# Kernel tuning notes

Measured on AMD Instinct MI355X. Metric: run time of the kernel, lower is better.

## Reference

```python
import jax, jax.numpy as jnp
import numpy as np

B, N, E, D, P = 128, 50000, 300000, 256, 8


def setup_inputs() -> dict:
    key = jax.random.key(0)
    ks = jax.random.split(key, 13)
    scale = 1.0 / np.sqrt(D)  # keep uniform-init logits numerically sane
    return {
        "instruction_batch": jax.random.normal(ks[0], (B, D), jnp.float32),
        "distribution": jax.random.uniform(ks[1], (N,), jnp.float32),
        "node_prop_similarities": jax.random.uniform(ks[2], (B, P), jnp.float32),
        "relation_similarity": jax.random.uniform(ks[3], (B,), jnp.float32),
        "node_attrs": jax.random.normal(ks[4], (N, D), jnp.float32),
        "edge_attrs": jax.random.normal(ks[5], (E, D), jnp.float32),
        "W_node_props": jax.random.uniform(ks[6], (P, D, D), jnp.float32) * scale,
        "W_edge": jax.random.uniform(ks[7], (D, D), jnp.float32) * scale,
        "w_node_score": jax.random.uniform(ks[8], (D,), jnp.float32) * scale,
        "w_rel_score": jax.random.uniform(ks[9], (D,), jnp.float32) * scale,
        "node_indices": jnp.sort(jax.random.randint(ks[10], (N,), 0, B)),
        "edge_batch_indices": jax.random.randint(ks[11], (E,), 0, B),
        "edge_indices": jax.random.randint(ks[12], (2, E), 0, N),
    }


def _segment_softmax(logits, seg, num_segments):
    # softmax over all entries sharing the same segment (= per-graph softmax)
    m = jax.ops.segment_max(logits, seg, num_segments=num_segments)
    e = jnp.exp(logits - m[seg])
    s = jax.ops.segment_sum(e, seg, num_segments=num_segments)
    return e / s[seg]


def reference(instruction_batch, distribution, node_prop_similarities,
              relation_similarity, node_attrs, edge_attrs,
              W_node_props, W_edge, w_node_score, w_rel_score,
              node_indices, edge_batch_indices, edge_indices):
    num_graphs = instruction_batch.shape[0]

    # node_scores[n,d] = elu( sum_p sim[n,p] * instr[n,d] * (W_p @ attr_n)[d] )
    sim_n = node_prop_similarities[node_indices]          # [N, P]
    instr_n = instruction_batch[node_indices]             # [N, D]
    wa = jnp.einsum("pde,ne->npd", W_node_props, node_attrs)  # [N, P, D]
    node_scores = jax.nn.elu(
        jnp.einsum("np,nd,npd->nd", sim_n, instr_n, wa))   # [N, D]

    # edge_scores[e,d] = elu( instr[batch(e),d] * (W_edge @ edge_attr_e)[d] )
    edge_scores = jax.nn.elu(
        instruction_batch[edge_batch_indices] * (edge_attrs @ W_edge.T))  # [E, D]

    # per-graph (sparse) softmax over node state logits
    state_logits = node_scores @ w_node_score              # [N]
    next_states = _segment_softmax(state_logits, node_indices, num_graphs)

    # scatter: aggregate weighted edge messages at destination nodes
    src, dst = edge_indices[0], edge_indices[1]
    msgs = distribution[src, None] * edge_scores           # [E, D]
    agg = jnp.zeros_like(node_scores).at[dst].add(msgs)    # [N, D]
    rel_logits = agg @ w_rel_score                         # [N]
    next_relations = _segment_softmax(rel_logits, node_indices, num_graphs)

    r = relation_similarity[node_indices]                  # [N]
    return r * next_relations + (1.0 - r) * next_states
```

## Files before the change

### kernel.cpp

```cpp
#include <hip/hip_runtime.h>

#define NB 128
#define NN 50000
#define NE 300000
#define ND 256
#define NP 8

typedef __attribute__((ext_vector_type(4))) float f32x4;
typedef __attribute__((ext_vector_type(8))) short s16x8;

__device__ __forceinline__ unsigned short bf16rtn(float f) {
    unsigned int u = __float_as_uint(f);
    unsigned int r = (u + 0x7fffu + ((u >> 16) & 1u)) >> 16;
    return (unsigned short)r;
}

__device__ __forceinline__ int cvtpk(float lo, float hi) {
    int r;
    asm("v_cvt_pk_bf16_f32 %0, %1, %2" : "=v"(r) : "v"(lo), "v"(hi));
    return r;
}

__device__ __forceinline__ s16x8 pack8(f32x4 a, f32x4 b) {
    union { int d[4]; s16x8 v; } u;
    u.d[0] = cvtpk(a[0], a[1]);
    u.d[1] = cvtpk(a[2], a[3]);
    u.d[2] = cvtpk(b[0], b[1]);
    u.d[3] = cvtpk(b[2], b[3]);
    return u.v;
}

__device__ __forceinline__ float eluf(float x) {
    return x > 0.f ? x : __expf(x) - 1.f;
}

__device__ __forceinline__ float rowsum16(float x) {
    int t;
    t = __builtin_amdgcn_update_dpp(0, __float_as_int(x), 0x121, 0xf, 0xf, true);
    x += __int_as_float(t);
    t = __builtin_amdgcn_update_dpp(0, __float_as_int(x), 0x122, 0xf, 0xf, true);
    x += __int_as_float(t);
    t = __builtin_amdgcn_update_dpp(0, __float_as_int(x), 0x124, 0xf, 0xf, true);
    x += __int_as_float(t);
    t = __builtin_amdgcn_update_dpp(0, __float_as_int(x), 0x128, 0xf, 0xf, true);
    x += __int_as_float(t);
    return x;
}

__device__ __forceinline__ void stage_W(char* Wl, const unsigned short* Wsrc,
                                        int tid, int nthr) {
    for (int i = tid; i < 8192; i += nthr) {
        int cg = i >> 9;
        int kk = (i >> 6) & 7;
        int ln = i & 63;
        const unsigned short* src =
            Wsrc + (size_t)(cg * 16 + (ln & 15)) * ND + kk * 32 + (ln >> 4) * 8;
        *(s16x8*)(Wl + i * 16) = *(const s16x8*)src;
    }
}

__global__ __launch_bounds__(256) void k_prep(
    const float* __restrict__ We, unsigned short* __restrict__ Wbf,
    const float* __restrict__ sim, const float* __restrict__ Wp,
    unsigned short* __restrict__ Weff,
    const int* __restrict__ nidx, int* __restrict__ starts,
    float* __restrict__ rel_logits,
    const int* __restrict__ eidx, const float* __restrict__ dist,
    float* __restrict__ dscg)
{
    int bid = blockIdx.x;
    int tid = threadIdx.x;
    if (bid < 64) {
        int i = (bid * 256 + tid) * 4;
        f32x4 v = *(const f32x4*)(We + i);
        Wbf[i + 0] = bf16rtn(v[0]); Wbf[i + 1] = bf16rtn(v[1]);
        Wbf[i + 2] = bf16rtn(v[2]); Wbf[i + 3] = bf16rtn(v[3]);
    } else if (bid < 320) {
        int wb = bid - 64;
        int chunk = (wb & 31) * 256 + tid;
        int off = chunk * 8;
        float wp[NP][8];
#pragma unroll
        for (int p = 0; p < NP; ++p) {
            const float* src = Wp + (size_t)p * ND * ND + off;
            f32x4 w0 = *(const f32x4*)src;
            f32x4 w1 = *(const f32x4*)(src + 4);
            wp[p][0] = w0[0]; wp[p][1] = w0[1]; wp[p][2] = w0[2]; wp[p][3] = w0[3];
            wp[p][4] = w1[0]; wp[p][5] = w1[1]; wp[p][6] = w1[2]; wp[p][7] = w1[3];
        }
        int b0 = (wb >> 5) * 16;
        for (int bb = 0; bb < 16; ++bb) {
            int b = b0 + bb;
            float g[8] = {0.f, 0.f, 0.f, 0.f, 0.f, 0.f, 0.f, 0.f};
#pragma unroll
            for (int p = 0; p < NP; ++p) {
                float s = sim[b * NP + p];
#pragma unroll
                for (int j = 0; j < 8; ++j) g[j] += s * wp[p][j];
            }
            s16x8 v;
#pragma unroll
            for (int j = 0; j < 8; ++j) v[j] = (short)bf16rtn(g[j]);
            *(s16x8*)(Weff + (size_t)b * ND * ND + off) = v;
        }
    } else {
        int n = (bid - 320) * 256 + tid;
        if (n < NE) dscg[n] = dist[eidx[n]];
        if (n >= NN) return;
        rel_logits[n] = 0.f;
        int cur = nidx[n];
        int prev = (n == 0) ? -1 : nidx[n - 1];
        for (int b2 = prev + 1; b2 <= cur; ++b2) starts[b2] = n;
        if (n == NN - 1)
            for (int b2 = cur + 1; b2 <= NB; ++b2) starts[b2] = NN;
    }
}

__global__ __launch_bounds__(1024, 4) void k_main(
    const float* __restrict__ instr, const float* __restrict__ dscg,
    const float* __restrict__ eattrs, const unsigned short* __restrict__ Wbf,
    const float* __restrict__ wrs, const int* __restrict__ ebidx,
    const int* __restrict__ eidx, float* __restrict__ rel_logits,
    const unsigned short* __restrict__ Weff, const float* __restrict__ nattrs,
    const float* __restrict__ wns, const int* __restrict__ starts,
    float* __restrict__ state_logits)
{
    __shared__ char Wl[131072];

    int tid = threadIdx.x;
    int lane = tid & 63;
    int wave = tid >> 6;
    int l15 = lane & 15;
    int q = lane >> 4;

    if (blockIdx.x < 256) {
        stage_W(Wl, Wbf, tid, 1024);
        __syncthreads();

        int gw = wave * 256 + blockIdx.x;
        const int NT = NE / 16;
        for (int t = gw; t < NT; t += 4096) {
            int e0 = t * 16;
            int e4 = e0 + 4 * q;
            int eb0 = ebidx[e4 + 0], eb1 = ebidx[e4 + 1];
            int eb2 = ebidx[e4 + 2], eb3 = ebidx[e4 + 3];
            float dv0 = dscg[e4 + 0], dv1 = dscg[e4 + 1];
            float dv2 = dscg[e4 + 2], dv3 = dscg[e4 + 3];
            int dd0 = eidx[NE + e4 + 0], dd1 = eidx[NE + e4 + 1];
            int dd2 = eidx[NE + e4 + 2], dd3 = eidx[NE + e4 + 3];

            const float* ib0 = instr + (size_t)eb0 * ND + l15;
            const float* ib1 = instr + (size_t)eb1 * ND + l15;
            const float* ib2 = instr + (size_t)eb2 * ND + l15;
            const float* ib3 = instr + (size_t)eb3 * ND + l15;

            const float* arow = eattrs + (size_t)(e0 + l15) * ND + q * 8;
            s16x8 afr[8];
#pragma unroll
            for (int kk = 0; kk < 8; ++kk) {
                f32x4 a0 = *(const f32x4*)(arow + kk * 32);
                f32x4 a1 = *(const f32x4*)(arow + kk * 32 + 4);
                afr[kk] = pack8(a0, a1);
            }

            float nv0 = ib0[0], nv1 = ib1[0], nv2 = ib2[0], nv3 = ib3[0];
            float nw = wrs[l15];

            float p0 = 0.f, p1 = 0.f, p2 = 0.f, p3 = 0.f;
#pragma unroll 1
            for (int cg = 0; cg < 16; ++cg) {
                float v0 = nv0, v1 = nv1, v2 = nv2, v3 = nv3, wvc = nw;
                int cn = (cg + 1 < 16 ? cg + 1 : 15) * 16;
                nv0 = ib0[cn]; nv1 = ib1[cn]; nv2 = ib2[cn]; nv3 = ib3[cn];
                nw = wrs[cn + l15];

                f32x4 acc = {0.f, 0.f, 0.f, 0.f};
                const char* fb = Wl + cg * 8192 + lane * 16;
                __builtin_amdgcn_s_setprio(1);
#pragma unroll
                for (int kk = 0; kk < 8; ++kk) {
                    s16x8 bf = *(const s16x8*)(fb + kk * 1024);
                    acc = __builtin_amdgcn_mfma_f32_16x16x32_bf16(afr[kk], bf, acc, 0, 0, 0);
                }
                __builtin_amdgcn_s_setprio(0);
                p0 += wvc * eluf(v0 * acc[0]);
                p1 += wvc * eluf(v1 * acc[1]);
                p2 += wvc * eluf(v2 * acc[2]);
                p3 += wvc * eluf(v3 * acc[3]);
            }
            p0 = rowsum16(p0); p1 = rowsum16(p1);
            p2 = rowsum16(p2); p3 = rowsum16(p3);
            if (l15 == 0) {
                atomicAdd(&rel_logits[dd0], dv0 * p0);
                atomicAdd(&rel_logits[dd1], dv1 * p1);
                atomicAdd(&rel_logits[dd2], dv2 * p2);
                atomicAdd(&rel_logits[dd3], dv3 * p3);
            }
        }
    } else {
        int nb = blockIdx.x - 256;
        int b = nb >> 1;
        int half = nb & 1;
        int s0 = starts[b], s1 = starts[b + 1];
        int nt = (s1 - s0 + 15) >> 4;

        stage_W(Wl, Weff + (size_t)b * ND * ND, tid, 1024);
        __syncthreads();

        const float* irow = instr + (size_t)b * ND + l15;
        for (int t = half * 16 + wave; t < nt; t += 32) {
            int n0 = s0 + t * 16;
            int arn = n0 + l15;
            bool valid = arn < s1;
            const float* arow = nattrs + (size_t)arn * ND + q * 8;
            s16x8 afr[8];
#pragma unroll
            for (int kk = 0; kk < 8; ++kk) {
                f32x4 a0 = {0.f, 0.f, 0.f, 0.f}, a1 = {0.f, 0.f, 0.f, 0.f};
                if (valid) {
                    a0 = *(const f32x4*)(arow + kk * 32);
                    a1 = *(const f32x4*)(arow + kk * 32 + 4);
                }
                afr[kk] = pack8(a0, a1);
            }

            float p0 = 0.f, p1 = 0.f, p2 = 0.f, p3 = 0.f;
#pragma unroll 1
            for (int cg = 0; cg < 16; ++cg) {
                f32x4 acc = {0.f, 0.f, 0.f, 0.f};
                const char* fb = Wl + cg * 8192 + lane * 16;
                __builtin_amdgcn_s_setprio(1);
#pragma unroll
                for (int kk = 0; kk < 8; ++kk) {
                    s16x8 bf = *(const s16x8*)(fb + kk * 1024);
                    acc = __builtin_amdgcn_mfma_f32_16x16x32_bf16(afr[kk], bf, acc, 0, 0, 0);
                }
                __builtin_amdgcn_s_setprio(0);
                int c = cg * 16;
                float ivc = irow[c];
                float wvc = wns[c + l15];
                p0 += wvc * eluf(ivc * acc[0]);
                p1 += wvc * eluf(ivc * acc[1]);
                p2 += wvc * eluf(ivc * acc[2]);
                p3 += wvc * eluf(ivc * acc[3]);
            }
            p0 = rowsum16(p0); p1 = rowsum16(p1);
            p2 = rowsum16(p2); p3 = rowsum16(p3);
            if (l15 == 0) {
                int n = n0 + 4 * q;
                if (n + 0 < s1) state_logits[n + 0] = p0;
                if (n + 1 < s1) state_logits[n + 1] = p1;
                if (n + 2 < s1) state_logits[n + 2] = p2;
                if (n + 3 < s1) state_logits[n + 3] = p3;
            }
        }
    }
}

__global__ __launch_bounds__(256) void k_softmax_mix(
    const float* __restrict__ state_l, const float* __restrict__ rel_l,
    const int* __restrict__ starts, const float* __restrict__ relsim,
    float* __restrict__ out)
{
    __shared__ float wms[4], wmr[4], wss[4], wsr[4];
    int b = blockIdx.x;
    int s0 = starts[b], s1 = starts[b + 1];
    if (s1 <= s0) return;
    int tid = threadIdx.x, lane = tid & 63, wave = tid >> 6;

    float ms = -3.4e38f, mr = -3.4e38f;
    for (int n = s0 + tid; n < s1; n += 256) {
        ms = fmaxf(ms, state_l[n]);
        mr = fmaxf(mr, rel_l[n]);
    }
#pragma unroll
    for (int m = 1; m < 64; m <<= 1) {
        ms = fmaxf(ms, __shfl_xor(ms, m, 64));
        mr = fmaxf(mr, __shfl_xor(mr, m, 64));
    }
    if (lane == 0) { wms[wave] = ms; wmr[wave] = mr; }
    __syncthreads();
    ms = fmaxf(fmaxf(wms[0], wms[1]), fmaxf(wms[2], wms[3]));
    mr = fmaxf(fmaxf(wmr[0], wmr[1]), fmaxf(wmr[2], wmr[3]));

    float ss = 0.f, sr = 0.f;
    for (int n = s0 + tid; n < s1; n += 256) {
        ss += __expf(state_l[n] - ms);
        sr += __expf(rel_l[n] - mr);
    }
#pragma unroll
    for (int m = 1; m < 64; m <<= 1) {
        ss += __shfl_xor(ss, m, 64);
        sr += __shfl_xor(sr, m, 64);
    }
    if (lane == 0) { wss[wave] = ss; wsr[wave] = sr; }
    __syncthreads();
    ss = wss[0] + wss[1] + wss[2] + wss[3];
    sr = wsr[0] + wsr[1] + wsr[2] + wsr[3];

    float rb = relsim[b];
    float iss = 1.f / ss, isr = 1.f / sr;
    for (int n = s0 + tid; n < s1; n += 256) {
        out[n] = rb * __expf(rel_l[n] - mr) * isr
               + (1.f - rb) * __expf(state_l[n] - ms) * iss;
    }
}

extern "C" void kernel_launch(void* const* d_in, const int* in_sizes, int n_in,
                              void* d_out, int out_size, void* d_ws, size_t ws_size,
                              hipStream_t stream) {
    const float* instr  = (const float*)d_in[0];
    const float* dist   = (const float*)d_in[1];
    const float* sim    = (const float*)d_in[2];
    const float* relsim = (const float*)d_in[3];
    const float* nattr  = (const float*)d_in[4];
    const float* eattr  = (const float*)d_in[5];
    const float* Wp     = (const float*)d_in[6];
    const float* We     = (const float*)d_in[7];
    const float* wns    = (const float*)d_in[8];
    const float* wrs    = (const float*)d_in[9];
    const int* nidx     = (const int*)d_in[10];
    const int* ebidx    = (const int*)d_in[11];
    const int* eidx     = (const int*)d_in[12];
    float* out = (float*)d_out;

    char* ws = (char*)d_ws;
    float* rel_logits   = (float*)ws;
    float* state_logits = rel_logits + NN;
    int* starts         = (int*)(ws + 400000);
    unsigned short* Wbf = (unsigned short*)(ws + 400640);
    unsigned short* Weff= (unsigned short*)(ws + 532480);
    float* dscg         = (float*)(ws + 17309696);

    k_prep<<<320 + (NE + 255) / 256, 256, 0, stream>>>(
        We, Wbf, sim, Wp, Weff, nidx, starts, rel_logits, eidx, dist, dscg);
    k_main<<<512, 1024, 0, stream>>>(instr, dscg, eattr, Wbf, wrs, ebidx, eidx,
                                     rel_logits, Weff, nattr, wns, starts,
                                     state_logits);
    k_softmax_mix<<<NB, 256, 0, stream>>>(state_logits, rel_logits, starts,
                                          relsim, out);
}
```

Before: 129.1 us.

## Process 32 edges per wave reusing each LDS weight fragment across two MFMAs

The edge path now handles two 16-edge tiles per wave iteration, so each B fragment read from LDS feeds two MFMA chains. Block size drops from 1024 to 512 threads and the node path's wave stride is adjusted to match. The software prefetch of instruction values across column groups is removed, so those gathers are issued inside the loop. The change trades higher register pressure and half as many waves for less LDS traffic per MFMA and more independent MFMA work per wave.

```diff
diff --git a/kernel.cpp b/kernel.cpp
--- a/kernel.cpp
+++ b/kernel.cpp
@@ -116,7 +116,7 @@
     }
 }
 
-__global__ __launch_bounds__(1024, 4) void k_main(
+__global__ __launch_bounds__(512, 2) void k_main(
     const float* __restrict__ instr, const float* __restrict__ dscg,
     const float* __restrict__ eattrs, const unsigned short* __restrict__ Wbf,
     const float* __restrict__ wrs, const int* __restrict__ ebidx,
@@ -134,67 +134,80 @@
     int q = lane >> 4;
 
     if (blockIdx.x < 256) {
-        stage_W(Wl, Wbf, tid, 1024);
+        stage_W(Wl, Wbf, tid, 512);
         __syncthreads();
 
         int gw = wave * 256 + blockIdx.x;
-        const int NT = NE / 16;
-        for (int t = gw; t < NT; t += 4096) {
-            int e0 = t * 16;
-            int e4 = e0 + 4 * q;
-            int eb0 = ebidx[e4 + 0], eb1 = ebidx[e4 + 1];
-            int eb2 = ebidx[e4 + 2], eb3 = ebidx[e4 + 3];
-            float dv0 = dscg[e4 + 0], dv1 = dscg[e4 + 1];
-            float dv2 = dscg[e4 + 2], dv3 = dscg[e4 + 3];
-            int dd0 = eidx[NE + e4 + 0], dd1 = eidx[NE + e4 + 1];
-            int dd2 = eidx[NE + e4 + 2], dd3 = eidx[NE + e4 + 3];
-
-            const float* ib0 = instr + (size_t)eb0 * ND + l15;
-            const float* ib1 = instr + (size_t)eb1 * ND + l15;
-            const float* ib2 = instr + (size_t)eb2 * ND + l15;
-            const float* ib3 = instr + (size_t)eb3 * ND + l15;
-
-            const float* arow = eattrs + (size_t)(e0 + l15) * ND + q * 8;
-            s16x8 afr[8];
+        const int NT = NE / 32;
+        for (int t = gw; t < NT; t += 2048) {
+            int e0 = t * 32;
+            int e4a = e0 + 4 * q;
+            int e4b = e0 + 16 + 4 * q;
+
+            const float* ib0 = instr + (size_t)ebidx[e4a + 0] * ND + l15;
+            const float* ib1 = instr + (size_t)ebidx[e4a + 1] * ND + l15;
+            const float* ib2 = instr + (size_t)ebidx[e4a + 2] * ND + l15;
+            const float* ib3 = instr + (size_t)ebidx[e4a + 3] * ND + l15;
+            const float* ib4 = instr + (size_t)ebidx[e4b + 0] * ND + l15;
+            const float* ib5 = instr + (size_t)ebidx[e4b + 1] * ND + l15;
+            const float* ib6 = instr + (size_t)ebidx[e4b + 2] * ND + l15;
+            const float* ib7 = instr + (size_t)ebidx[e4b + 3] * ND + l15;
+
+            const float* ar0 = eattrs + (size_t)(e0 + l15) * ND + q * 8;
+            const float* ar1 = ar0 + 16 * ND;
+            s16x8 af0[8], af1[8];
 #pragma unroll
             for (int kk = 0; kk < 8; ++kk) {
-                f32x4 a0 = *(const f32x4*)(arow + kk * 32);
-                f32x4 a1 = *(const f32x4*)(arow + kk * 32 + 4);
-                afr[kk] = pack8(a0, a1);
-            }
-
-            float nv0 = ib0[0], nv1 = ib1[0], nv2 = ib2[0], nv3 = ib3[0];
-            float nw = wrs[l15];
+                f32x4 a0 = *(const f32x4*)(ar0 + kk * 32);
+                f32x4 a1 = *(const f32x4*)(ar0 + kk * 32 + 4);
+                af0[kk] = pack8(a0, a1);
+            }
+#pragma unroll
+            for (int kk = 0; kk < 8; ++kk) {
+                f32x4 a0 = *(const f32x4*)(ar1 + kk * 32);
+                f32x4 a1 = *(const f32x4*)(ar1 + kk * 32 + 4);
+                af1[kk] = pack8(a0, a1);
+            }
 
             float p0 = 0.f, p1 = 0.f, p2 = 0.f, p3 = 0.f;
+            float p4 = 0.f, p5 = 0.f, p6 = 0.f, p7 = 0.f;
 #pragma unroll 1
             for (int cg = 0; cg < 16; ++cg) {
-                float v0 = nv0, v1 = nv1, v2 = nv2, v3 = nv3, wvc = nw;
-                int cn = (cg + 1 < 16 ? cg + 1 : 15) * 16;
-                nv0 = ib0[cn]; nv1 = ib1[cn]; nv2 = ib2[cn]; nv3 = ib3[cn];
-                nw = wrs[cn + l15];
-
-                f32x4 acc = {0.f, 0.f, 0.f, 0.f};
+                f32x4 acc0 = {0.f, 0.f, 0.f, 0.f};
+                f32x4 acc1 = {0.f, 0.f, 0.f, 0.f};
                 const char* fb = Wl + cg * 8192 + lane * 16;
                 __builtin_amdgcn_s_setprio(1);
 #pragma unroll
                 for (int kk = 0; kk < 8; ++kk) {
                     s16x8 bf = *(const s16x8*)(fb + kk * 1024);
-                    acc = __builtin_amdgcn_mfma_f32_16x16x32_bf16(afr[kk], bf, acc, 0, 0, 0);
+                    acc0 = __builtin_amdgcn_mfma_f32_16x16x32_bf16(af0[kk], bf, acc0, 0, 0, 0);
+                    acc1 = __builtin_amdgcn_mfma_f32_16x16x32_bf16(af1[kk], bf, acc1, 0, 0, 0);
                 }
                 __builtin_amdgcn_s_setprio(0);
-                p0 += wvc * eluf(v0 * acc[0]);
-                p1 += wvc * eluf(v1 * acc[1]);
-                p2 += wvc * eluf(v2 * acc[2]);
-                p3 += wvc * eluf(v3 * acc[3]);
+                int c = cg * 16;
+                float wvc = wrs[c + l15];
+                p0 += wvc * eluf(ib0[c] * acc0[0]);
+                p1 += wvc * eluf(ib1[c] * acc0[1]);
+                p2 += wvc * eluf(ib2[c] * acc0[2]);
+                p3 += wvc * eluf(ib3[c] * acc0[3]);
+                p4 += wvc * eluf(ib4[c] * acc1[0]);
+                p5 += wvc * eluf(ib5[c] * acc1[1]);
+                p6 += wvc * eluf(ib6[c] * acc1[2]);
+                p7 += wvc * eluf(ib7[c] * acc1[3]);
             }
             p0 = rowsum16(p0); p1 = rowsum16(p1);
             p2 = rowsum16(p2); p3 = rowsum16(p3);
+            p4 = rowsum16(p4); p5 = rowsum16(p5);
+            p6 = rowsum16(p6); p7 = rowsum16(p7);
             if (l15 == 0) {
-                atomicAdd(&rel_logits[dd0], dv0 * p0);
-                atomicAdd(&rel_logits[dd1], dv1 * p1);
-                atomicAdd(&rel_logits[dd2], dv2 * p2);
-                atomicAdd(&rel_logits[dd3], dv3 * p3);
+                atomicAdd(&rel_logits[eidx[NE + e4a + 0]], dscg[e4a + 0] * p0);
+                atomicAdd(&rel_logits[eidx[NE + e4a + 1]], dscg[e4a + 1] * p1);
+                atomicAdd(&rel_logits[eidx[NE + e4a + 2]], dscg[e4a + 2] * p2);
+                atomicAdd(&rel_logits[eidx[NE + e4a + 3]], dscg[e4a + 3] * p3);
+                atomicAdd(&rel_logits[eidx[NE + e4b + 0]], dscg[e4b + 0] * p4);
+                atomicAdd(&rel_logits[eidx[NE + e4b + 1]], dscg[e4b + 1] * p5);
+                atomicAdd(&rel_logits[eidx[NE + e4b + 2]], dscg[e4b + 2] * p6);
+                atomicAdd(&rel_logits[eidx[NE + e4b + 3]], dscg[e4b + 3] * p7);
             }
         }
     } else {
@@ -204,11 +217,11 @@
         int s0 = starts[b], s1 = starts[b + 1];
         int nt = (s1 - s0 + 15) >> 4;
 
-        stage_W(Wl, Weff + (size_t)b * ND * ND, tid, 1024);
+        stage_W(Wl, Weff + (size_t)b * ND * ND, tid, 512);
         __syncthreads();
 
         const float* irow = instr + (size_t)b * ND + l15;
-        for (int t = half * 16 + wave; t < nt; t += 32) {
+        for (int t = half * 8 + wave; t < nt; t += 16) {
             int n0 = s0 + t * 16;
             int arn = n0 + l15;
             bool valid = arn < s1;
@@ -334,9 +347,9 @@
 
     k_prep<<<320 + (NE + 255) / 256, 256, 0, stream>>>(
         We, Wbf, sim, Wp, Weff, nidx, starts, rel_logits, eidx, dist, dscg);
-    k_main<<<512, 1024, 0, stream>>>(instr, dscg, eattr, Wbf, wrs, ebidx, eidx,
-                                     rel_logits, Weff, nattr, wns, starts,
-                                     state_logits);
+    k_main<<<512, 512, 0, stream>>>(instr, dscg, eattr, Wbf, wrs, ebidx, eidx,
+                                    rel_logits, Weff, nattr, wns, starts,
+                                    state_logits);
     k_softmax_mix<<<NB, 256, 0, stream>>>(state_logits, rel_logits, starts,
                                           relsim, out);
 }
```

New measurement: 150.2 us. +16.3%, slower.
